# Performance work log

Hardware: AMD Instinct MI355X
Metric: run time of the kernel (lower is better)

Reference implementation:

```python
import itertools
import jax, jax.numpy as jnp
import numpy as np

EPS = 1e-15
B, K, H, W = 64, 8, 128, 128


def setup_inputs() -> dict:
    key = jax.random.key(0)
    k1, k2 = jax.random.split(key)
    pred_masks = jax.random.uniform(k1, (B, K, H, W), dtype=jnp.float32)
    aug_masks = jax.random.uniform(k2, (B, K, H, W), dtype=jnp.float32)
    return {"pred_masks": pred_masks, "aug_masks": aug_masks}


def _mask_kl_div(pred, true):
    # true * (log(true+eps) - log(pred+eps)), mean over (H, W)
    return (true * (jnp.log(true + EPS) - jnp.log(pred + EPS))).mean(axis=(-2, -1))


# all K! permutations, precomputed once (K=8 -> 40320 perms)
_PERMS = jnp.asarray(np.array(list(itertools.permutations(range(K))), dtype=np.int32))


def reference(pred_masks, aug_masks):
    b, k, h, w = pred_masks.shape
    t = aug_masks  # targets are detached in torch for the cost matrix
    # Fused pairwise KL cost matrix (avoids the (B,K,K,H,W) broadcast):
    # C[b,i,j] = mean_hw[ t_j*log(t_j+eps) ] - mean_hw[ t_j*log(p_i+eps) ]
    ent = (t * jnp.log(t + EPS)).mean(axis=(-2, -1))          # (B, K) over j
    cross = jnp.einsum('bjhw,bihw->bij', t, jnp.log(pred_masks + EPS)) / (h * w)
    C = ent[:, None, :] - cross                                # (B, K, K)
    # exact linear assignment via exhaustive search over K! permutations
    rows = jnp.arange(k)
    costs = C[:, rows[None, :], _PERMS].sum(axis=-1)           # (B, K!)
    R2C = _PERMS[jnp.argmin(costs, axis=1)]                    # (B, K) col for each row
    # permute rows: out[b, i] = pred[b, argsort(R2C)[b, i]]
    row_perm = jnp.argsort(R2C, axis=1)
    pred_perm = jnp.take_along_axis(pred_masks, row_perm[:, :, None, None], axis=1)
    l = _mask_kl_div(pred_perm, t)                             # (B, K)
    return l.mean(), pred_perm[..., None]
```

## Files before the change

kernel.cpp:

```cpp
#include <hip/hip_runtime.h>


#define BB 64
#define KK 8
#define HW 16384
#define EPSF 1e-15f

struct MaskTab {
    unsigned char masks[255];
    int off[9];
};

constexpr MaskTab make_tab() {
    MaskTab t{};
    int idx = 0;
    for (int p = 1; p <= 8; ++p) {
        t.off[p - 1] = idx;
        for (int m = 1; m < 256; ++m) {
            int c = 0;
            for (int b = 0; b < 8; ++b) c += (m >> b) & 1;
            if (c == p) t.masks[idx++] = (unsigned char)m;
        }
    }
    t.off[8] = idx;
    return t;
}

__constant__ MaskTab kTab = make_tab();

__device__ __forceinline__ float dot4(float4 t, float4 l) {
    return t.x * l.x + t.y * l.y + t.z * l.z + t.w * l.w;
}

__device__ __forceinline__ float4 log4(float4 a) {
    float4 r;
    r.x = __logf(a.x + EPSF); r.y = __logf(a.y + EPSF);
    r.z = __logf(a.z + EPSF); r.w = __logf(a.w + EPSF);
    return r;
}

__global__ __launch_bounds__(256) void cost_kernel(const float* __restrict__ pred,
                                                   const float* __restrict__ aug,
                                                   float* __restrict__ part,
                                                   float* __restrict__ out)
{
    __shared__ float red[4][9];

    const int p    = blockIdx.x;
    const int i    = p >> 6;
    const int b    = p & 63;
    const int tid  = threadIdx.x;
    const int wave = tid >> 6;
    const int lane = tid & 63;

    if (p == 0 && tid == 0) out[0] = 0.f;

    const float* prow  = pred + ((size_t)b * KK + i) * HW;
    const float* abase = aug  + (size_t)b * KK * HW;

    float acc[8];
#pragma unroll
    for (int j = 0; j < 8; ++j) acc[j] = 0.f;
    float eacc = 0.f;

    const int rot = p & 15;

    for (int m = 0; m < 16; ++m) {
        const int mm = (m + rot) & 15;
        const int e  = (tid + 256 * mm) * 4;

        const float4 pq = *(const float4*)(prow + e);
        const float4 la = log4(pq);

#pragma unroll
        for (int j = 0; j < 8; ++j) {
            const float4 a = *(const float4*)(abase + (size_t)j * HW + e);
            acc[j] += dot4(a, la);
            if (j == i) eacc += dot4(a, log4(a));
        }
    }

#pragma unroll
    for (int r = 0; r < 3; ++r) {
        const int d    = 1 << r;
        const int half = 4 >> r;
        const bool hi  = (lane & d) != 0;
#pragma unroll
        for (int k = 0; k < half; ++k) {
            const float send = hi ? acc[k] : acc[k + half];
            const float recv = __shfl_xor(send, d);
            acc[k] = (hi ? acc[k + half] : acc[k]) + recv;
        }
    }
    float av = acc[0];
    av += __shfl_xor(av, 8);
    av += __shfl_xor(av, 16);
    av += __shfl_xor(av, 32);

#pragma unroll
    for (int d = 1; d < 64; d <<= 1) eacc += __shfl_xor(eacc, d);

    if (lane < 8)
        red[wave][((lane & 1) << 2) | (lane & 2) | ((lane & 4) >> 2)] = av;
    if (lane == 0)
        red[wave][8] = eacc;
    __syncthreads();

    if (tid < 9)
        part[(size_t)p * 9 + tid] = red[0][tid] + red[1][tid] + red[2][tid] + red[3][tid];
}

__global__ __launch_bounds__(256) void permute_kernel(const float* __restrict__ pred,
                                                      const float* __restrict__ part,
                                                      float* __restrict__ out)
{
    __shared__ float C[64];
    __shared__ float dp[256];
    __shared__ int   choice[256];
    __shared__ int   inv8[8];

    const int p    = blockIdx.x;
    const int b    = p >> 3;
    const int tid  = threadIdx.x;

    if (tid < 64) {
        const int ii = tid >> 3, jj = tid & 7;
        const float cross = part[((size_t)ii * 64 + b) * 9 + jj];
        const float entj  = part[((size_t)jj * 64 + b) * 9 + 8];
        C[tid] = entj - cross;
    }
    if (tid == 0) dp[0] = 0.f;
    __syncthreads();

    const int grp = tid >> 3;
    const int j   = tid & 7;
    for (int lvl = 1; lvl <= 8; ++lvl) {
        const int start = kTab.off[lvl - 1];
        const int end   = kTab.off[lvl];
        const float* Crow = &C[(lvl - 1) * 8];
        for (int bse = start; bse < end; bse += 32) {
            const int mi = bse + grp;
            if (mi < end) {
                const int M = kTab.masks[mi];
                float v  = 1e30f;
                int   bj = 0;
                if (M & (1 << j)) {
                    v  = dp[M ^ (1 << j)] + Crow[j];
                    bj = j;
                }
#pragma unroll
                for (int d = 1; d < 8; d <<= 1) {
                    const float ov = __shfl_xor(v, d);
                    const int   oj = __shfl_xor(bj, d);
                    if (ov < v) { v = ov; bj = oj; }
                }
                if (j == 0) { dp[M] = v; choice[M] = bj; }
            }
        }
        __syncthreads();
    }

    if (tid == 0) {
        int mask = 255;
        for (int r = 7; r >= 0; --r) {
            const int jj = choice[mask];
            inv8[jj] = r;
            mask ^= 1 << jj;
        }
        if ((p & 7) == 0)
            atomicAdd(out, dp[255] * (1.0f / (16384.0f * 512.0f)));
    }
    __syncthreads();

    const int src_row = inv8[p & 7];
    const float* src  = pred + ((size_t)(b << 3) + src_row) * HW;
    float*      drow  = out + 1 + (size_t)p * HW;

#pragma unroll
    for (int m = 0; m < 16; ++m) {
        const int f = tid + 256 * m;
        const int e = 3 + 4 * f;
        if (f < 4095) {
            float4 v;
            v.x = src[e]; v.y = src[e + 1]; v.z = src[e + 2]; v.w = src[e + 3];
            *(float4*)(drow + e) = v;
        } else {
            drow[0] = src[0]; drow[1] = src[1]; drow[2] = src[2];
            drow[16383] = src[16383];
        }
    }
}

extern "C" void kernel_launch(void* const* d_in, const int* in_sizes, int n_in,
                              void* d_out, int out_size, void* d_ws, size_t ws_size,
                              hipStream_t stream) {
    const float* pred = (const float*)d_in[0];
    const float* aug  = (const float*)d_in[1];
    float* out  = (float*)d_out;
    float* part = (float*)d_ws;

    cost_kernel<<<dim3(512), dim3(256), 0, stream>>>(pred, aug, part, out);
    permute_kernel<<<dim3(512), dim3(256), 0, stream>>>(pred, part, out);
}
```

Baseline: 121.6 us.

## Fuse cost and permute kernels with per-batch atomic counters and spin-waits

Merges the cost-matrix kernel and the assignment/permute kernel into one launch. The last block to finish for each batch runs the bitmask DP and publishes the inverse permutation; the other blocks for that batch spin-wait on a per-batch counter before copying their permuted row. Block 0 waits for all batches and reduces the loss itself instead of using atomicAdd on the output. The aug loads are batched ahead of the log math with a sched barrier, and the rotation is keyed on batch index. This removes a launch and the global round trip between kernels, but relies on all 512 blocks being co-resident (launch_bounds 256,2) to avoid deadlock, and the counters persist across calls through epoch arithmetic.

New measurement: 184.7 us. 1.52x slower.

```diff
diff --git a/kernel.cpp b/kernel.cpp
--- a/kernel.cpp
+++ b/kernel.cpp
@@ -28,6 +28,13 @@
 
 __constant__ MaskTab kTab = make_tab();
 
+__device__ int   g_cnt[64];
+__device__ int   g_done[64];
+__device__ int   g_all;
+__device__ float g_part[512 * 9];
+__device__ float g_loss[64];
+__device__ int   g_invtab[64][8];
+
 __device__ __forceinline__ float dot4(float4 t, float4 l) {
     return t.x * l.x + t.y * l.y + t.z * l.z + t.w * l.w;
 }
@@ -39,12 +46,15 @@
     return r;
 }
 
-__global__ __launch_bounds__(256) void cost_kernel(const float* __restrict__ pred,
-                                                   const float* __restrict__ aug,
-                                                   float* __restrict__ part,
-                                                   float* __restrict__ out)
+__global__ __launch_bounds__(256, 2) void fused_kernel(const float* __restrict__ pred,
+                                                       const float* __restrict__ aug,
+                                                       float* __restrict__ out)
 {
     __shared__ float red[4][9];
+    __shared__ int   sE, sLast;
+    __shared__ float C[64];
+    __shared__ float dp[256];
+    __shared__ int   choice[256];
 
     const int p    = blockIdx.x;
     const int i    = p >> 6;
@@ -53,8 +63,6 @@
     const int wave = tid >> 6;
     const int lane = tid & 63;
 
-    if (p == 0 && tid == 0) out[0] = 0.f;
-
     const float* prow  = pred + ((size_t)b * KK + i) * HW;
     const float* abase = aug  + (size_t)b * KK * HW;
 
@@ -63,20 +71,24 @@
     for (int j = 0; j < 8; ++j) acc[j] = 0.f;
     float eacc = 0.f;
 
-    const int rot = p & 15;
+    const int rot = b & 15;
 
     for (int m = 0; m < 16; ++m) {
         const int mm = (m + rot) & 15;
         const int e  = (tid + 256 * mm) * 4;
 
         const float4 pq = *(const float4*)(prow + e);
+        float4 a[8];
+#pragma unroll
+        for (int j = 0; j < 8; ++j)
+            a[j] = *(const float4*)(abase + (size_t)j * HW + e);
+        __builtin_amdgcn_sched_barrier(0);
+
         const float4 la = log4(pq);
-
 #pragma unroll
         for (int j = 0; j < 8; ++j) {
-            const float4 a = *(const float4*)(abase + (size_t)j * HW + e);
-            acc[j] += dot4(a, la);
-            if (j == i) eacc += dot4(a, log4(a));
+            acc[j] += dot4(a[j], la);
+            if (j == i) eacc += dot4(a[j], log4(a[j]));
         }
     }
 
@@ -107,74 +119,83 @@
     __syncthreads();
 
     if (tid < 9)
-        part[(size_t)p * 9 + tid] = red[0][tid] + red[1][tid] + red[2][tid] + red[3][tid];
-}
-
-__global__ __launch_bounds__(256) void permute_kernel(const float* __restrict__ pred,
-                                                      const float* __restrict__ part,
-                                                      float* __restrict__ out)
-{
-    __shared__ float C[64];
-    __shared__ float dp[256];
-    __shared__ int   choice[256];
-    __shared__ int   inv8[8];
-
-    const int p    = blockIdx.x;
-    const int b    = p >> 3;
-    const int tid  = threadIdx.x;
-
-    if (tid < 64) {
-        const int ii = tid >> 3, jj = tid & 7;
-        const float cross = part[((size_t)ii * 64 + b) * 9 + jj];
-        const float entj  = part[((size_t)jj * 64 + b) * 9 + 8];
-        C[tid] = entj - cross;
-    }
-    if (tid == 0) dp[0] = 0.f;
-    __syncthreads();
-
-    const int grp = tid >> 3;
-    const int j   = tid & 7;
-    for (int lvl = 1; lvl <= 8; ++lvl) {
-        const int start = kTab.off[lvl - 1];
-        const int end   = kTab.off[lvl];
-        const float* Crow = &C[(lvl - 1) * 8];
-        for (int bse = start; bse < end; bse += 32) {
-            const int mi = bse + grp;
-            if (mi < end) {
-                const int M = kTab.masks[mi];
-                float v  = 1e30f;
-                int   bj = 0;
-                if (M & (1 << j)) {
-                    v  = dp[M ^ (1 << j)] + Crow[j];
-                    bj = j;
+        g_part[(size_t)p * 9 + tid] = red[0][tid] + red[1][tid] + red[2][tid] + red[3][tid];
+    __threadfence();
+    __syncthreads();
+
+    if (tid == 0) {
+        const int old = atomicAdd(&g_cnt[b], 1);
+        sLast = ((old & 7) == 7);
+        sE    = old >> 3;
+    }
+    __syncthreads();
+
+    if (sLast) {
+        __threadfence();
+
+        if (tid < 64) {
+            const int ii = tid >> 3, jj = tid & 7;
+            const float cross = g_part[((size_t)ii * 64 + b) * 9 + jj];
+            const float entj  = g_part[((size_t)jj * 64 + b) * 9 + 8];
+            C[tid] = entj - cross;
+        }
+        if (tid == 0) dp[0] = 0.f;
+        __syncthreads();
+
+        const int grp = tid >> 3;
+        const int j   = tid & 7;
+        for (int lvl = 1; lvl <= 8; ++lvl) {
+            const int start = kTab.off[lvl - 1];
+            const int end   = kTab.off[lvl];
+            const float* Crow = &C[(lvl - 1) * 8];
+            for (int bse = start; bse < end; bse += 32) {
+                const int mi = bse + grp;
+                if (mi < end) {
+                    const int M = kTab.masks[mi];
+                    float v  = 1e30f;
+                    int   bj = 0;
+                    if (M & (1 << j)) {
+                        v  = dp[M ^ (1 << j)] + Crow[j];
+                        bj = j;
+                    }
+#pragma unroll
+                    for (int d = 1; d < 8; d <<= 1) {
+                        const float ov = __shfl_xor(v, d);
+                        const int   oj = __shfl_xor(bj, d);
+                        if (ov < v) { v = ov; bj = oj; }
+                    }
+                    if (j == 0) { dp[M] = v; choice[M] = bj; }
                 }
-#pragma unroll
-                for (int d = 1; d < 8; d <<= 1) {
-                    const float ov = __shfl_xor(v, d);
-                    const int   oj = __shfl_xor(bj, d);
-                    if (ov < v) { v = ov; bj = oj; }
-                }
-                if (j == 0) { dp[M] = v; choice[M] = bj; }
             }
+            __syncthreads();
+        }
+
+        if (tid == 0) {
+            int mask = 255;
+            for (int r = 7; r >= 0; --r) {
+                const int jj = choice[mask];
+                g_invtab[b][jj] = r;
+                mask ^= 1 << jj;
+            }
+            g_loss[b] = dp[255];
+            __threadfence();
+            atomicAdd(&g_done[b], 1);
+            atomicAdd(&g_all, 1);
         }
         __syncthreads();
     }
 
     if (tid == 0) {
-        int mask = 255;
-        for (int r = 7; r >= 0; --r) {
-            const int jj = choice[mask];
-            inv8[jj] = r;
-            mask ^= 1 << jj;
-        }
-        if ((p & 7) == 0)
-            atomicAdd(out, dp[255] * (1.0f / (16384.0f * 512.0f)));
-    }
-    __syncthreads();
-
-    const int src_row = inv8[p & 7];
+        const int E = sE;
+        while (atomicAdd(&g_done[b], 0) <= E)
+            __builtin_amdgcn_s_sleep(16);
+    }
+    __syncthreads();
+    __threadfence();
+
+    const int src_row = g_invtab[b][i];
     const float* src  = pred + ((size_t)(b << 3) + src_row) * HW;
-    float*      drow  = out + 1 + (size_t)p * HW;
+    float*      drow  = out + 1 + ((size_t)(b << 3) + i) * HW;
 
 #pragma unroll
     for (int m = 0; m < 16; ++m) {
@@ -189,6 +210,22 @@
             drow[16383] = src[16383];
         }
     }
+
+    if (p == 0) {
+        if (tid == 0) {
+            const int target = 64 * (sE + 1);
+            while (atomicAdd(&g_all, 0) < target)
+                __builtin_amdgcn_s_sleep(16);
+        }
+        __syncthreads();
+        __threadfence();
+        if (tid < 64) {
+            float lv = g_loss[tid];
+#pragma unroll
+            for (int d = 1; d < 64; d <<= 1) lv += __shfl_xor(lv, d);
+            if (tid == 0) out[0] = lv * (1.0f / (16384.0f * 512.0f));
+        }
+    }
 }
 
 extern "C" void kernel_launch(void* const* d_in, const int* in_sizes, int n_in,
@@ -196,9 +233,7 @@
                               hipStream_t stream) {
     const float* pred = (const float*)d_in[0];
     const float* aug  = (const float*)d_in[1];
-    float* out  = (float*)d_out;
-    float* part = (float*)d_ws;
-
-    cost_kernel<<<dim3(512), dim3(256), 0, stream>>>(pred, aug, part, out);
-    permute_kernel<<<dim3(512), dim3(256), 0, stream>>>(pred, part, out);
-}
+    float* out = (float*)d_out;
+
+    fused_kernel<<<dim3(512), dim3(256), 0, stream>>>(pred, aug, out);
+}
```
